# Optimization experiments

Hardware: AMD Instinct MI355X
Metric: run time of the kernel (lower is better)

The kernel has to match this reference:

```python
import jax, jax.numpy as jnp
import numpy as np

GRID_RES = 64          # grid_resolution
N_POINTS = 1_048_576   # 4 * 64^3
BATCH = 4
CHANNELS = 64
IMG = 512              # image_resolution = round(K[0,0])


def setup_inputs() -> dict:
    key = jax.random.key(0)
    k1, k2, k3 = jax.random.split(key, 3)
    batch_ids = jax.random.randint(k1, (N_POINTS, 1), 0, BATCH)
    grid_ijk = jax.random.randint(k2, (N_POINTS, 3), 0, GRID_RES)
    dense_coords = jnp.concatenate([batch_ids, grid_ijk], axis=1).astype(jnp.int32)
    pixel_features = jax.random.normal(k3, (BATCH, CHANNELS, IMG, IMG), dtype=jnp.float32)
    K = jnp.array([[512.0, 0.0, 256.0],
                   [0.0, 512.0, 256.0],
                   [0.0, 0.0, 1.0]], dtype=jnp.float32)
    P = jnp.array([[1.0, 0.0, 0.0, 0.0],
                   [0.0, 1.0, 0.0, 0.0],
                   [0.0, 0.0, 1.0, 3.0],
                   [0.0, 0.0, 0.0, 1.0]], dtype=jnp.float32)
    return {"dense_coords": dense_coords, "pixel_features": pixel_features, "K": K, "P": P}


def reference(dense_coords, pixel_features, K, P):
    # grid coords -> world positions in [-1, 1]
    batch_ids = dense_coords[:, 0]
    grid_pos = dense_coords[:, 1:].astype(pixel_features.dtype)
    world = grid_pos * (2.0 / (GRID_RES - 1)) - 1.0            # [N,3]

    # camera projection: P (4x4 world->camera), K (3x3 intrinsics)
    ones = jnp.ones((world.shape[0], 1), dtype=world.dtype)
    pts_h = jnp.concatenate([world, ones], axis=1)             # [N,4]
    cam = pts_h @ P.T                                          # [N,4]
    cam = cam / cam[:, 3:4]
    img_h = cam[:, :3] @ K.T                                   # [N,3]
    img = img_h[:, :2] / img_h[:, 2:3]                         # [N,2] (x, y)
    points_depth = cam[:, 2:3]                                 # [N,1]

    # bilinear gather weights (i = row = y, j = col = x, matching torch code)
    y_real = img[:, 1]
    x_real = img[:, 0]
    i_f = jnp.floor(y_real)
    j_f = jnp.floor(x_real)
    di = (y_real - i_f)[:, None]                               # [N,1]
    dj = (x_real - j_f)[:, None]
    H, W = pixel_features.shape[2], pixel_features.shape[3]
    i0 = jnp.clip(i_f.astype(jnp.int32), 0, H - 1)
    i1 = jnp.clip(i_f.astype(jnp.int32) + 1, 0, H - 1)
    j0 = jnp.clip(j_f.astype(jnp.int32), 0, W - 1)
    j1 = jnp.clip(j_f.astype(jnp.int32) + 1, 0, W - 1)

    # irregular gathers: pixel_features[b, :, i, j] -> [N, C]
    f00 = pixel_features[batch_ids, :, i0, j0]
    f10 = pixel_features[batch_ids, :, i1, j0]
    f01 = pixel_features[batch_ids, :, i0, j1]
    f11 = pixel_features[batch_ids, :, i1, j1]

    mean_j = (1.0 - di) * f00 + di * f10
    mean_jp = (1.0 - di) * f01 + di * f11
    feature_bilinear = (1.0 - dj) * mean_j + dj * mean_jp      # [N,C]
    return feature_bilinear, points_depth
```

## Files before the change

kernel.cpp:

```cpp
#include <hip/hip_runtime.h>
#include <hip/hip_fp16.h>
#include <stdint.h>

#define GRID_RES 64
#define NPTS 1048576
#define CH 64
#define IMG 512
#define BATCH 4
#define NBINS 1024
#define NBLK_D (NPTS / 4)
#define CHUNKS_PER_XCD (NBLK_D / 8)

struct Rec { float di, dj; uint32_t meta, pt; };

__device__ __forceinline__ void project_point(
    const int4 cd, const float* __restrict__ Km, const float* __restrict__ Pm,
    float& di, float& dj, int& i0, int& i1, int& j0, int& j1, int& b, float& cz_out)
{
    b = cd.x;
    const float s = 2.0f / (GRID_RES - 1);
    float wx = (float)cd.y * s - 1.0f;
    float wy = (float)cd.z * s - 1.0f;
    float wz = (float)cd.w * s - 1.0f;

    float cx = Pm[0]*wx  + Pm[1]*wy  + Pm[2]*wz  + Pm[3];
    float cy = Pm[4]*wx  + Pm[5]*wy  + Pm[6]*wz  + Pm[7];
    float cz = Pm[8]*wx  + Pm[9]*wy  + Pm[10]*wz + Pm[11];
    float cw = Pm[12]*wx + Pm[13]*wy + Pm[14]*wz + Pm[15];
    cx = cx / cw; cy = cy / cw; cz = cz / cw;

    float ix = Km[0]*cx + Km[1]*cy + Km[2]*cz;
    float iy = Km[3]*cx + Km[4]*cy + Km[5]*cz;
    float iz = Km[6]*cx + Km[7]*cy + Km[8]*cz;
    float x = ix / iz;
    float y = iy / iz;

    float fi = floorf(y);
    float fj = floorf(x);
    di = y - fi;
    dj = x - fj;
    i0 = min(max((int)fi, 0), IMG - 1);
    i1 = min(max((int)fi + 1, 0), IMG - 1);
    j0 = min(max((int)fj, 0), IMG - 1);
    j1 = min(max((int)fj + 1, 0), IMG - 1);
    cz_out = cz;
}


__global__ __launch_bounds__(256) void pass_transpose_h(
    const float* __restrict__ feat, __half* __restrict__ featT)
{
    __shared__ __half lds[128 * 68];
    const int t   = threadIdx.x;
    const int blk = blockIdx.x;
    const int q = blk & 3;
    const int i = (blk >> 2) & 511;
    const int b = blk >> 11;
    const int j0 = q << 7;

    const int px2 = (t & 63) << 1;
    const int c0  = (t >> 6) << 1;
    const float* src = feat + ((size_t)(b * CH + c0) << 18)
                            + ((size_t)i << 9) + j0 + px2;
    #pragma unroll
    for (int k = 0; k < 8; ++k) {
        const float* s0 = src + ((size_t)(k * 8) << 18);
        float2 v0 = *(const float2*)(s0);
        float2 v1 = *(const float2*)(s0 + (1u << 18));
        int cc = c0 + k * 8;
        *(__half2*)&lds[(px2 + 0) * 68 + cc] = __floats2half2_rn(v0.x, v1.x);
        *(__half2*)&lds[(px2 + 1) * 68 + cc] = __floats2half2_rn(v0.y, v1.y);
    }
    __syncthreads();

    const int c4    = (t & 15) << 2;
    const int pbase = t >> 4;
    __half* dst = featT + ((size_t)b << 24) + ((size_t)i << 15)
                        + ((size_t)j0 << 6) + c4;
    #pragma unroll
    for (int m = 0; m < 8; ++m) {
        int pix = pbase + (m << 4);
        *(uint2*)(dst + ((size_t)pix << 6)) = *(const uint2*)&lds[pix * 68 + c4];
    }
}

__global__ __launch_bounds__(256, 4) void pass_gather_h(
    const int* __restrict__ coords, const float* __restrict__ Km,
    const float* __restrict__ Pm, const __half* __restrict__ featT,
    float* __restrict__ out_feat, float* __restrict__ out_depth)
{
    const uint32_t wave = blockIdx.x * 4u + (threadIdx.x >> 6);
    const uint32_t p0 = wave << 6;
    const int lane = threadIdx.x & 63;
    const int c = lane;

    const int4 cd = ((const int4*)coords)[p0 + lane];
    float di, dj, cz; int i0, i1, j0, j1, b;
    project_point(cd, Km, Pm, di, dj, i0, i1, j0, j1, b, cz);
    out_depth[p0 + lane] = cz;

    uint32_t meta = ((uint32_t)b << 20) | ((uint32_t)i0 << 11) | ((uint32_t)j0 << 2)
                  | ((uint32_t)(i1 - i0) << 1) | (uint32_t)(j1 - j0);
    uint32_t dib = __float_as_uint(di);
    uint32_t djb = __float_as_uint(dj);

    float* outp = out_feat + (((size_t)p0) << 6) + c;

    #pragma unroll
    for (int u = 0; u < 64; ++u) {
        uint32_t m  = __builtin_amdgcn_readlane(meta, u);
        float diu = __uint_as_float(__builtin_amdgcn_readlane(dib, u));
        float dju = __uint_as_float(__builtin_amdgcn_readlane(djb, u));
        int j1d = m & 1;
        int i1d = (m >> 1) & 1;
        uint32_t off = ((m >> 2) & 511u) << 6;
        off += ((m >> 11) & 511u) << 15;
        off += (m >> 20) << 24;
        const __half* base = featT + off + c;
        float f00 = __half2float(base[0]);
        float f01 = __half2float(base[j1d << 6]);
        float f10 = __half2float(base[i1d << 15]);
        float f11 = __half2float(base[(i1d << 15) + (j1d << 6)]);
        float omdi = 1.0f - diu;
        float mj  = omdi * f00 + diu * f10;
        float mjp = omdi * f01 + diu * f11;
        outp[(size_t)u << 6] = (1.0f - dju) * mj + dju * mjp;
    }
}


__global__ void pass_zero(uint32_t* counts) {
    counts[threadIdx.x] = 0;
}

__global__ __launch_bounds__(256) void pass_hist(
    const int* __restrict__ coords, const float* __restrict__ Km,
    const float* __restrict__ Pm, uint32_t* __restrict__ counts,
    Rec* __restrict__ tmp, float* __restrict__ out_depth)
{
    __shared__ uint32_t h[NBINS];
    for (int i = threadIdx.x; i < NBINS; i += 256) h[i] = 0;
    __syncthreads();

    int pt = blockIdx.x * 256 + threadIdx.x;
    const int4 cd = ((const int4*)coords)[pt];
    float di, dj, cz; int i0, i1, j0, j1, b;
    project_point(cd, Km, Pm, di, dj, i0, i1, j0, j1, b, cz);

    Rec r;
    r.di = di; r.dj = dj;
    r.meta = ((uint32_t)b << 20) | ((uint32_t)i0 << 11) | ((uint32_t)j0 << 2)
           | ((uint32_t)(i1 - i0) << 1) | (uint32_t)(j1 - j0);
    r.pt = (uint32_t)pt;
    tmp[pt] = r;
    out_depth[pt] = cz;

    int bin = (b << 8) | ((i0 >> 5) << 4) | (j0 >> 5);
    atomicAdd(&h[bin], 1u);
    __syncthreads();
    for (int i = threadIdx.x; i < NBINS; i += 256)
        if (h[i]) atomicAdd(&counts[i], h[i]);
}

__global__ void pass_scan(const uint32_t* __restrict__ counts, uint32_t* __restrict__ cursor) {
    __shared__ uint32_t a[NBINS];
    int t = threadIdx.x;
    a[t] = counts[t];
    __syncthreads();
    for (int off = 1; off < NBINS; off <<= 1) {
        uint32_t v = a[t];
        uint32_t add = (t >= off) ? a[t - off] : 0u;
        __syncthreads();
        a[t] = v + add;
        __syncthreads();
    }
    cursor[t] = (t == 0) ? 0u : a[t - 1];
}

__global__ __launch_bounds__(256) void pass_scatter(
    const Rec* __restrict__ tmp, uint32_t* __restrict__ cursor, Rec* __restrict__ recs)
{
    int pt = blockIdx.x * 256 + threadIdx.x;
    Rec r = tmp[pt];
    int i0 = (r.meta >> 11) & 511;
    int j0 = (r.meta >> 2) & 511;
    int b  = r.meta >> 20;
    int bin = (b << 8) | ((i0 >> 5) << 4) | (j0 >> 5);
    uint32_t pos = atomicAdd(&cursor[bin], 1u);
    recs[pos] = r;
}

__global__ __launch_bounds__(256) void pass_gather(
    const Rec* __restrict__ recs, const float* __restrict__ feat,
    float* __restrict__ out_feat)
{
    uint32_t bi = blockIdx.x;
    uint32_t chunk = (bi & 7u) * CHUNKS_PER_XCD + (bi >> 3);
    uint32_t p = chunk * 4u + (threadIdx.x >> 6);
    int c = threadIdx.x & 63;

    Rec r = recs[p];
    int j1d = r.meta & 1;
    int i1d = (r.meta >> 1) & 1;
    int j0  = (r.meta >> 2) & 511;
    int i0  = (r.meta >> 11) & 511;
    int b   = r.meta >> 20;

    const float* base = feat + ((size_t)(b * CH + c) << 18);
    const float* r0 = base + (i0 << 9);
    const float* r1 = r0 + (i1d << 9);
    float f00 = r0[j0];
    float f01 = r0[j0 + j1d];
    float f10 = r1[j0];
    float f11 = r1[j0 + j1d];

    float omdi = 1.0f - r.di;
    float mj  = omdi * f00 + r.di * f10;
    float mjp = omdi * f01 + r.di * f11;
    float res = (1.0f - r.dj) * mj + r.dj * mjp;

    out_feat[(size_t)r.pt * CH + c] = res;
}

__global__ __launch_bounds__(256) void gs_tok(
    const int* __restrict__ coords, const float* __restrict__ feat,
    const float* __restrict__ Km, const float* __restrict__ Pm,
    float* __restrict__ out_feat, float* __restrict__ out_depth)
{
    int t = blockIdx.x * blockDim.x + threadIdx.x;
    int point = t >> 6;
    int c = t & 63;
    if (point >= NPTS) return;
    const int4 cd = ((const int4*)coords)[point];
    float di, dj, cz; int i0, i1, j0, j1, b;
    project_point(cd, Km, Pm, di, dj, i0, i1, j0, j1, b, cz);
    const float* base = feat + ((size_t)(b * CH + c) << 18);
    const float* r0 = base + (i0 << 9);
    const float* r1 = base + (i1 << 9);
    float f00 = r0[j0], f01 = r0[j1], f10 = r1[j0], f11 = r1[j1];
    float omdi = 1.0f - di;
    float mj  = omdi * f00 + di * f10;
    float mjp = omdi * f01 + di * f11;
    float res = (1.0f - dj) * mj + dj * mjp;
    out_feat[(size_t)point * CH + c] = res;
    if (c == 0) out_depth[point] = cz;
}

extern "C" void kernel_launch(void* const* d_in, const int* in_sizes, int n_in,
                              void* d_out, int out_size, void* d_ws, size_t ws_size,
                              hipStream_t stream)
{
    const int*   coords = (const int*)d_in[0];
    const float* feat   = (const float*)d_in[1];
    const float* Km     = (const float*)d_in[2];
    const float* Pm     = (const float*)d_in[3];
    float* out_feat  = (float*)d_out;
    float* out_depth = (float*)d_out + (size_t)NPTS * CH;

    const size_t featT_sz = (size_t)BATCH * CH * IMG * IMG * sizeof(__half);

    if (ws_size >= featT_sz) {
        __half* featT = (__half*)d_ws;
        pass_transpose_h<<<BATCH * IMG * (IMG / 128), 256, 0, stream>>>(feat, featT);
        pass_gather_h<<<NPTS / 256, 256, 0, stream>>>(
            coords, Km, Pm, featT, out_feat, out_depth);
        return;
    }

    const size_t counts_off = 0;
    const size_t cursor_off = 4096;
    const size_t tmp2_off   = 16384;
    const size_t recs_off   = 16384 + (size_t)NPTS * sizeof(Rec);
    const size_t need_old   = recs_off + (size_t)NPTS * sizeof(Rec);

    if (ws_size >= need_old) {
        uint32_t* counts = (uint32_t*)((char*)d_ws + counts_off);
        uint32_t* cursor = (uint32_t*)((char*)d_ws + cursor_off);
        Rec*      tmp    = (Rec*)((char*)d_ws + tmp2_off);
        Rec*      recs   = (Rec*)((char*)d_ws + recs_off);

        pass_zero<<<1, NBINS, 0, stream>>>(counts);
        pass_hist<<<NPTS / 256, 256, 0, stream>>>(coords, Km, Pm, counts, tmp, out_depth);
        pass_scan<<<1, NBINS, 0, stream>>>(counts, cursor);
        pass_scatter<<<NPTS / 256, 256, 0, stream>>>(tmp, cursor, recs);
        pass_gather<<<NBLK_D, 256, 0, stream>>>(recs, feat, out_feat);
        return;
    }

    const long long total = (long long)NPTS * 64;
    gs_tok<<<(int)((total + 255) / 256), 256, 0, stream>>>(
        coords, feat, Km, Pm, out_feat, out_depth);
}
```

Measured before the change: 548.3 us.

## Fuse transpose and gather into one cooperative persistent kernel with grid sync

Result: slower. 849.4 us (+54.9%).

```diff
diff --git a/kernel.cpp b/kernel.cpp
--- a/kernel.cpp
+++ b/kernel.cpp
@@ -1,5 +1,6 @@
 #include <hip/hip_runtime.h>
 #include <hip/hip_fp16.h>
+#include <hip/hip_cooperative_groups.h>
 #include <stdint.h>
 
 #define GRID_RES 64
@@ -7,6 +8,9 @@
 #define CH 64
 #define IMG 512
 #define BATCH 4
+#define NTILES (BATCH * IMG * (IMG / 128))
+#define NGROUPS (NPTS / 256)
+#define COOP_GRID 2048
 #define NBINS 1024
 #define NBLK_D (NPTS / 4)
 #define CHUNKS_PER_XCD (NBLK_D / 8)
@@ -47,12 +51,10 @@
 }
 
 
-__global__ __launch_bounds__(256) void pass_transpose_h(
-    const float* __restrict__ feat, __half* __restrict__ featT)
-{
-    __shared__ __half lds[128 * 68];
-    const int t   = threadIdx.x;
-    const int blk = blockIdx.x;
+__device__ __forceinline__ void transpose_tile(
+    const float* __restrict__ feat, __half* __restrict__ featT,
+    __half* lds, int blk, int t)
+{
     const int q = blk & 3;
     const int i = (blk >> 2) & 511;
     const int b = blk >> 11;
@@ -82,16 +84,15 @@
         int pix = pbase + (m << 4);
         *(uint2*)(dst + ((size_t)pix << 6)) = *(const uint2*)&lds[pix * 68 + c4];
     }
-}
-
-__global__ __launch_bounds__(256, 4) void pass_gather_h(
+    __syncthreads();
+}
+
+__device__ __forceinline__ void gather_group64(
     const int* __restrict__ coords, const float* __restrict__ Km,
     const float* __restrict__ Pm, const __half* __restrict__ featT,
-    float* __restrict__ out_feat, float* __restrict__ out_depth)
-{
-    const uint32_t wave = blockIdx.x * 4u + (threadIdx.x >> 6);
-    const uint32_t p0 = wave << 6;
-    const int lane = threadIdx.x & 63;
+    float* __restrict__ out_feat, float* __restrict__ out_depth,
+    uint32_t p0, int lane)
+{
     const int c = lane;
 
     const int4 cd = ((const int4*)coords)[p0 + lane];
@@ -128,6 +129,46 @@
     }
 }
 
+__global__ __launch_bounds__(256, 8) void fused_all(
+    const int* __restrict__ coords, const float* __restrict__ Km,
+    const float* __restrict__ Pm, const float* __restrict__ feat,
+    __half* __restrict__ featT, float* __restrict__ out_feat,
+    float* __restrict__ out_depth)
+{
+    __shared__ __half lds[128 * 68];
+    const int t = threadIdx.x;
+    const int G = gridDim.x;
+
+    for (int blk = blockIdx.x; blk < NTILES; blk += G)
+        transpose_tile(feat, featT, lds, blk, t);
+
+    cooperative_groups::this_grid().sync();
+
+    const int w = t >> 6;
+    const int lane = t & 63;
+    for (uint32_t g = blockIdx.x; g < NGROUPS; g += G) {
+        uint32_t p0 = (g << 8) + ((uint32_t)w << 6);
+        gather_group64(coords, Km, Pm, featT, out_feat, out_depth, p0, lane);
+    }
+}
+
+__global__ __launch_bounds__(256) void pass_transpose_h(
+    const float* __restrict__ feat, __half* __restrict__ featT)
+{
+    __shared__ __half lds[128 * 68];
+    transpose_tile(feat, featT, lds, blockIdx.x, threadIdx.x);
+}
+
+__global__ __launch_bounds__(256, 4) void pass_gather_h(
+    const int* __restrict__ coords, const float* __restrict__ Km,
+    const float* __restrict__ Pm, const __half* __restrict__ featT,
+    float* __restrict__ out_feat, float* __restrict__ out_depth)
+{
+    const uint32_t wave = blockIdx.x * 4u + (threadIdx.x >> 6);
+    gather_group64(coords, Km, Pm, featT, out_feat, out_depth,
+                   wave << 6, threadIdx.x & 63);
+}
+
 
 __global__ void pass_zero(uint32_t* counts) {
     counts[threadIdx.x] = 0;
@@ -261,7 +302,16 @@
 
     if (ws_size >= featT_sz) {
         __half* featT = (__half*)d_ws;
-        pass_transpose_h<<<BATCH * IMG * (IMG / 128), 256, 0, stream>>>(feat, featT);
+
+        void* args[] = {
+            (void*)&coords, (void*)&Km, (void*)&Pm, (void*)&feat,
+            (void*)&featT, (void*)&out_feat, (void*)&out_depth
+        };
+        hipError_t e = hipLaunchCooperativeKernel(
+            (const void*)fused_all, dim3(COOP_GRID), dim3(256), args, 0, stream);
+        if (e == hipSuccess) return;
+
+        pass_transpose_h<<<NTILES, 256, 0, stream>>>(feat, featT);
         pass_gather_h<<<NPTS / 256, 256, 0, stream>>>(
             coords, Km, Pm, featT, out_feat, out_depth);
         return;
```
